# Kernel tuning notes

Hardware: AMD Instinct MI355X
Metric: run time of the kernel (lower is better)

## Reference

```python
import jax, jax.numpy as jnp
import numpy as np

BS, C, H, W = 64, 3, 512, 512
DROP_PIX = 0.3          # fraction of pixels dropped
NOISE_STD = 0.1         # gaussian multiplicative noise std
RNG_SEED = 42           # internal forward randomness (torch RNG analog)


def setup_inputs() -> dict:
    key = jax.random.key(0)
    x = jax.random.normal(key, (BS, C, H, W), dtype=jnp.float32)
    return {"x": x}


def reference(x):
    bs, c, h, w = x.shape
    hw = h * w
    len_keep = int(hw * (1.0 - DROP_PIX))
    k_mask, k_noise = jax.random.split(jax.random.key(RNG_SEED))

    # Per-sample random permutation of pixel indices, keep first len_keep.
    # argsort of iid uniforms == uniformly random permutation (all bs at once,
    # replacing the Python loop + per-iteration randperm of the original).
    u = jax.random.uniform(k_mask, (bs, hw))
    keep_idx = jnp.argsort(u, axis=1)[:, :len_keep]          # [bs, len_keep]
    mask = jnp.zeros((bs, hw), dtype=x.dtype)
    mask = mask.at[jnp.arange(bs)[:, None], keep_idx].set(1.0)
    mask = mask.reshape(bs, 1, h, w)

    # drop_type == 'zeros'
    x = x * mask

    # additive_noise: gaussian multiplicative noise (real-valued branch)
    noise = jax.random.normal(k_noise, x.shape, dtype=x.dtype) * NOISE_STD + 1.0
    x = x * noise
    return x, mask
```

## Files before the change

kernel.cpp:

```cpp
#include <hip/hip_runtime.h>

typedef unsigned int u32;
typedef unsigned long long u64;
typedef unsigned char u8;

__host__ __device__ __forceinline__ void tf2x32(u32 k0, u32 k1, u32 x0, u32 x1,
                                                u32& o0, u32& o1)
{
    const u32 ks2 = k0 ^ k1 ^ 0x1BD11BDAu;
    x0 += k0; x1 += k1;
#define TF_R(r) { x0 += x1; x1 = (x1 << (r)) | (x1 >> (32 - (r))); x1 ^= x0; }
    TF_R(13) TF_R(15) TF_R(26) TF_R(6)
    x0 += k1; x1 += ks2 + 1u;
    TF_R(17) TF_R(29) TF_R(16) TF_R(24)
    x0 += ks2; x1 += k0 + 2u;
    TF_R(13) TF_R(15) TF_R(26) TF_R(6)
    x0 += k0; x1 += k1 + 3u;
    TF_R(17) TF_R(29) TF_R(16) TF_R(24)
    x0 += k1; x1 += ks2 + 4u;
    TF_R(13) TF_R(15) TF_R(26) TF_R(6)
    x0 += ks2; x1 += k0 + 5u;
#undef TF_R
    o0 = x0; o1 = x1;
}

__device__ __forceinline__ u32 rbits(u32 k0, u32 k1, u32 e)
{
    u32 o0, o1; tf2x32(k0, k1, 0u, e, o0, o1); return o0 ^ o1;
}

#define HW        262144u
#define PMASK     262143u
#define KEEP      183500u
#define NX        50331648u
#define NM        16777216u
#define NWORD     524288u
#define LO_F      (-0.99999994039535522461f)

#define WLO       5806464u
#define WWIDTH    131072u
#define NBIN      4096
#define ROWCAP    6144
#define BLKCAP    512

#define BITM_B    (NWORD * 4u)
#define CAND_B    (64u * ROWCAP * 8u)
#define WS_BYTES  (BITM_B + CAND_B)

__device__ u32 g_bitm[NWORD];
__device__ u64 g_cand[64 * ROWCAP];
__device__ u32 g_cnts[128];

__device__ __forceinline__ float noise_from_bits(u32 bits)
{
    float f  = __uint_as_float((bits >> 9) | 0x3F800000u) - 1.0f;
    float un = fmaf(f, 2.0f, LO_F);
    un = fmaxf(LO_F, un);
    float w = -__logf(fmaf(-un, un, 1.0f));
    float p;
    if (w < 5.0f) {
        w -= 2.5f;
        p = 2.81022636e-08f;
        p = fmaf(p, w, 3.43273939e-07f);
        p = fmaf(p, w, -3.5233877e-06f);
        p = fmaf(p, w, -4.39150654e-06f);
        p = fmaf(p, w, 0.00021858087f);
        p = fmaf(p, w, -0.00125372503f);
        p = fmaf(p, w, -0.00417768164f);
        p = fmaf(p, w, 0.246640727f);
        p = fmaf(p, w, 1.50140941f);
    } else {
        w = __fsqrt_rn(w) - 3.0f;
        p = -0.000200214257f;
        p = fmaf(p, w, 0.000100950558f);
        p = fmaf(p, w, 0.00134934322f);
        p = fmaf(p, w, -0.00367342844f);
        p = fmaf(p, w, 0.00573950773f);
        p = fmaf(p, w, -0.0076224613f);
        p = fmaf(p, w, 0.00943887047f);
        p = fmaf(p, w, 1.00167406f);
        p = fmaf(p, w, 2.83297682f);
    }
    float ei = p * un;
    return fmaf(1.41421356f * ei, 0.1f, 1.0f);
}

__global__ __launch_bounds__(256) void k1_scan(u32 mk0, u32 mk1,
                                               u32* __restrict__ bitm,
                                               u64* __restrict__ cand)
{
    __shared__ u64 s_cand[BLKCAP];
    __shared__ u32 s_cnt, s_below, s_base;
    const int t = threadIdx.x;
    const u32 l = (u32)t & 63u;
    const u32 w = (u32)t >> 6;
    const u32 blk = blockIdx.x;
    const u32 row = blk >> 4;
    const u32 base = blk << 14;
    if (t == 0) { s_cnt = 0; s_below = 0; }
    __syncthreads();
    u32 below = 0;
#pragma unroll 1
    for (int i = 0; i < 16; ++i) {
        const u32 base0 = base + ((u32)i << 10) + (w << 8);
        u64 bal[4];
#pragma unroll
        for (int j = 0; j < 4; ++j) {
            u32 e = base0 + ((u32)j << 6) + l;
            u32 m = rbits(mk0, mk1, e) >> 9;
            u32 d = m - WLO;
            below += d >> 31;
            bal[j] = __ballot((int)(d >> 31));
            if (d < WWIDTH) {
                u32 pos = atomicAdd(&s_cnt, 1u);
                if (pos < BLKCAP) s_cand[pos] = ((u64)m << 18) | (u64)(e & PMASK);
            }
        }
        if (l < 8u) {
            u32 qi = l >> 1;
            u64 b = (qi == 0u) ? bal[0] : (qi == 1u) ? bal[1]
                  : (qi == 2u) ? bal[2] : bal[3];
            u32 wv = (l & 1u) ? (u32)(b >> 32) : (u32)b;
            bitm[(base0 >> 5) + l] = wv;
        }
    }
    atomicAdd(&s_below, below);
    __syncthreads();
    u32 cnt = s_cnt; if (cnt > BLKCAP) cnt = BLKCAP;
    if (t == 0) {
        atomicAdd(&g_cnts[row], s_below);
        s_base = atomicAdd(&g_cnts[64 + row], cnt);
    }
    __syncthreads();
    u32 gbase = s_base;
    for (u32 i = (u32)t; i < cnt; i += 256u) {
        u32 gi = gbase + i;
        if (gi < ROWCAP) cand[row * ROWCAP + gi] = s_cand[i];
    }
}

__global__ __launch_bounds__(256) void k2_select(const u64* __restrict__ cand,
                                                 u32* __restrict__ bitm)
{
    __shared__ u32 h[NBIN];
    __shared__ u32 sh[258];
    __shared__ u64 tie[64];
    __shared__ u32 tiecnt;
    __shared__ u64 s_kst;
    const int t = threadIdx.x;
    const u32 row = blockIdx.x;
    u32 n = g_cnts[64 + row]; if (n > ROWCAP) n = ROWCAP;
    u32 below = g_cnts[row];
    u32 r = KEEP - below;
#pragma unroll
    for (int i = 0; i < NBIN / 256; ++i) h[t + (i << 8)] = 0;
    if (t == 0) tiecnt = 0;
    __syncthreads();
    const u64* rc = cand + row * ROWCAP;
    for (u32 i = (u32)t; i < n; i += 256u) {
        u32 m = (u32)(rc[i] >> 18);
        atomicAdd(&h[(m - WLO) >> 5], 1u);
    }
    __syncthreads();
    u32 v[16]; u32 s = 0;
#pragma unroll
    for (int i = 0; i < 16; ++i) { v[i] = h[t * 16 + i]; s += v[i]; }
    sh[t] = s;
    __syncthreads();
    if (t == 0) {
        u32 run = 0; u32 c = 0;
        for (; c < 255u; ++c) { u32 cs = sh[c]; if (run + cs >= r) break; run += cs; }
        sh[256] = c; sh[257] = run;
    }
    __syncthreads();
    u32 c = sh[256];
    if (t == (int)c) {
        u32 run = sh[257];
        u32 b = (u32)t * 16u + 15u; u32 r2 = r - run;
#pragma unroll
        for (int i = 0; i < 16; ++i) {
            if (run + v[i] >= r) { b = (u32)t * 16u + (u32)i; r2 = r - run; break; }
            run += v[i];
        }
        sh[256] = b; sh[257] = r2;
    }
    __syncthreads();
    u32 bstar = sh[256], r2 = sh[257];
    u32 mlo = WLO + (bstar << 5), mhi = mlo + 32u;
    for (u32 i = (u32)t; i < n; i += 256u) {
        u64 k = rc[i];
        u32 m = (u32)(k >> 18);
        if (m >= mlo && m < mhi) {
            u32 pos = atomicAdd(&tiecnt, 1u);
            if (pos < 64u) tie[pos] = k;
        }
    }
    __syncthreads();
    if (t == 0) {
        u32 cnt = tiecnt; if (cnt > 64u) cnt = 64u;
        if (r2 > cnt) r2 = cnt;
        u64 kst = 0;
        for (u32 it = 0; it < r2; ++it) {
            u64 mn = ~0ull; u32 mi = 0;
            for (u32 i2 = 0; i2 < cnt; ++i2) if (tie[i2] < mn) { mn = tie[i2]; mi = i2; }
            kst = mn; tie[mi] = ~0ull;
        }
        s_kst = kst;
    }
    __syncthreads();
    u64 kst = s_kst;
    for (u32 i = (u32)t; i < n; i += 256u) {
        u64 k = rc[i];
        if (k <= kst) {
            u32 p = (u32)k & PMASK;
            atomicOr(&bitm[(row << 13) + (p >> 5)], 1u << (p & 31u));
        }
    }
    if (t == 0) {
        g_cnts[row] = 0;
        g_cnts[64 + row] = 0;
    }
}

__global__ __launch_bounds__(256) void k34_final(const float4* __restrict__ x4,
                                                 float4* __restrict__ out4,
                                                 float4* __restrict__ mask4,
                                                 const u32* __restrict__ bitm,
                                                 u32 nk0, u32 nk1)
{
    u32 tid = blockIdx.x * 256u + threadIdx.x;
    u32 wrd = bitm[tid >> 3];
    u32 nib = wrd >> ((tid & 7u) << 2);
    float4 mk;
    mk.x = (nib & 1u) ? 1.0f : 0.0f;
    mk.y = (nib & 2u) ? 1.0f : 0.0f;
    mk.z = (nib & 4u) ? 1.0f : 0.0f;
    mk.w = (nib & 8u) ? 1.0f : 0.0f;
    mask4[tid] = mk;

    u32 row = tid >> 16;
    u32 p = (tid << 2) & PMASK;
    u32 b3 = row * 3u;
#pragma unroll
    for (u32 cc = 0; cc < 3u; ++cc) {
        u32 en = ((b3 + cc) << 18) | p;
        float4 xv = x4[en >> 2];
        float4 r;
        r.x = (xv.x * mk.x) * noise_from_bits(rbits(nk0, nk1, en));
        r.y = (xv.y * mk.y) * noise_from_bits(rbits(nk0, nk1, en + 1u));
        r.z = (xv.z * mk.z) * noise_from_bits(rbits(nk0, nk1, en + 2u));
        r.w = (xv.w * mk.w) * noise_from_bits(rbits(nk0, nk1, en + 3u));
        out4[en >> 2] = r;
    }
}

extern "C" void kernel_launch(void* const* d_in, const int* in_sizes, int n_in,
                              void* d_out, int out_size, void* d_ws, size_t ws_size,
                              hipStream_t stream) {
    const float* x = (const float*)d_in[0];
    float* xout = (float*)d_out;
    float* maskf = xout + NX;

    u32 mk0, mk1, nk0, nk1;
    tf2x32(0u, 42u, 0u, 0u, mk0, mk1);
    tf2x32(0u, 42u, 0u, 1u, nk0, nk1);

    u32* bitm; u64* cand;
    if (d_ws != nullptr && ws_size >= (size_t)WS_BYTES) {
        u8* wsp = (u8*)d_ws;
        bitm = (u32*)wsp;
        cand = (u64*)(wsp + BITM_B);
    } else {
        hipGetSymbolAddress((void**)&bitm, HIP_SYMBOL(g_bitm));
        hipGetSymbolAddress((void**)&cand, HIP_SYMBOL(g_cand));
    }

    k1_scan<<<1024, 256, 0, stream>>>(mk0, mk1, bitm, cand);
    k2_select<<<64, 256, 0, stream>>>(cand, bitm);
    k34_final<<<16384, 256, 0, stream>>>((const float4*)x, (float4*)xout,
                                         (float4*)maskf, bitm, nk0, nk1);
    (void)in_sizes; (void)n_in; (void)out_size;
}
```

Before: 475.1 us.

## Write float mask in scan/select kernels and use nontemporal loads/stores in final

The float mask output is now written directly by the scan kernel (below-threshold pixels) and by the select kernel (chosen tie candidates), so the final kernel no longer writes it. The final kernel also switches to nontemporal vector loads and stores for x and the output. This spreads the mask write traffic into the earlier, compute-bound RNG scan and aims to cut cache pollution in the streaming kernel. In exchange, the scan kernel issues scalar 4-byte stores, and the select kernel adds scattered stores.

New measurement: 510.7 us. +7.5%, slower.

```diff
diff --git a/kernel.cpp b/kernel.cpp
--- a/kernel.cpp
+++ b/kernel.cpp
@@ -3,6 +3,7 @@
 typedef unsigned int u32;
 typedef unsigned long long u64;
 typedef unsigned char u8;
+typedef float f32x4 __attribute__((ext_vector_type(4)));
 
 __host__ __device__ __forceinline__ void tf2x32(u32 k0, u32 k1, u32 x0, u32 x1,
                                                 u32& o0, u32& o1)
@@ -87,7 +88,8 @@
 
 __global__ __launch_bounds__(256) void k1_scan(u32 mk0, u32 mk1,
                                                u32* __restrict__ bitm,
-                                               u64* __restrict__ cand)
+                                               u64* __restrict__ cand,
+                                               float* __restrict__ maskf)
 {
     __shared__ u64 s_cand[BLKCAP];
     __shared__ u32 s_cnt, s_below, s_base;
@@ -109,8 +111,10 @@
             u32 e = base0 + ((u32)j << 6) + l;
             u32 m = rbits(mk0, mk1, e) >> 9;
             u32 d = m - WLO;
-            below += d >> 31;
-            bal[j] = __ballot((int)(d >> 31));
+            u32 blo = d >> 31;
+            below += blo;
+            bal[j] = __ballot((int)blo);
+            __builtin_nontemporal_store(blo ? 1.0f : 0.0f, &maskf[e]);
             if (d < WWIDTH) {
                 u32 pos = atomicAdd(&s_cnt, 1u);
                 if (pos < BLKCAP) s_cand[pos] = ((u64)m << 18) | (u64)(e & PMASK);
@@ -140,7 +144,8 @@
 }
 
 __global__ __launch_bounds__(256) void k2_select(const u64* __restrict__ cand,
-                                                 u32* __restrict__ bitm)
+                                                 u32* __restrict__ bitm,
+                                                 float* __restrict__ maskf)
 {
     __shared__ u32 h[NBIN];
     __shared__ u32 sh[258];
@@ -214,6 +219,7 @@
         if (k <= kst) {
             u32 p = (u32)k & PMASK;
             atomicOr(&bitm[(row << 13) + (p >> 5)], 1u << (p & 31u));
+            maskf[(row << 18) | p] = 1.0f;
         }
     }
     if (t == 0) {
@@ -222,21 +228,18 @@
     }
 }
 
-__global__ __launch_bounds__(256) void k34_final(const float4* __restrict__ x4,
-                                                 float4* __restrict__ out4,
-                                                 float4* __restrict__ mask4,
+__global__ __launch_bounds__(256) void k34_final(const f32x4* __restrict__ x4,
+                                                 f32x4* __restrict__ out4,
                                                  const u32* __restrict__ bitm,
                                                  u32 nk0, u32 nk1)
 {
     u32 tid = blockIdx.x * 256u + threadIdx.x;
     u32 wrd = bitm[tid >> 3];
     u32 nib = wrd >> ((tid & 7u) << 2);
-    float4 mk;
-    mk.x = (nib & 1u) ? 1.0f : 0.0f;
-    mk.y = (nib & 2u) ? 1.0f : 0.0f;
-    mk.z = (nib & 4u) ? 1.0f : 0.0f;
-    mk.w = (nib & 8u) ? 1.0f : 0.0f;
-    mask4[tid] = mk;
+    float mx = (nib & 1u) ? 1.0f : 0.0f;
+    float my = (nib & 2u) ? 1.0f : 0.0f;
+    float mz = (nib & 4u) ? 1.0f : 0.0f;
+    float mw = (nib & 8u) ? 1.0f : 0.0f;
 
     u32 row = tid >> 16;
     u32 p = (tid << 2) & PMASK;
@@ -244,13 +247,13 @@
 #pragma unroll
     for (u32 cc = 0; cc < 3u; ++cc) {
         u32 en = ((b3 + cc) << 18) | p;
-        float4 xv = x4[en >> 2];
-        float4 r;
-        r.x = (xv.x * mk.x) * noise_from_bits(rbits(nk0, nk1, en));
-        r.y = (xv.y * mk.y) * noise_from_bits(rbits(nk0, nk1, en + 1u));
-        r.z = (xv.z * mk.z) * noise_from_bits(rbits(nk0, nk1, en + 2u));
-        r.w = (xv.w * mk.w) * noise_from_bits(rbits(nk0, nk1, en + 3u));
-        out4[en >> 2] = r;
+        f32x4 xv = __builtin_nontemporal_load(&x4[en >> 2]);
+        f32x4 r;
+        r.x = (xv.x * mx) * noise_from_bits(rbits(nk0, nk1, en));
+        r.y = (xv.y * my) * noise_from_bits(rbits(nk0, nk1, en + 1u));
+        r.z = (xv.z * mz) * noise_from_bits(rbits(nk0, nk1, en + 2u));
+        r.w = (xv.w * mw) * noise_from_bits(rbits(nk0, nk1, en + 3u));
+        __builtin_nontemporal_store(r, &out4[en >> 2]);
     }
 }
 
@@ -275,9 +278,9 @@
         hipGetSymbolAddress((void**)&cand, HIP_SYMBOL(g_cand));
     }
 
-    k1_scan<<<1024, 256, 0, stream>>>(mk0, mk1, bitm, cand);
-    k2_select<<<64, 256, 0, stream>>>(cand, bitm);
-    k34_final<<<16384, 256, 0, stream>>>((const float4*)x, (float4*)xout,
-                                         (float4*)maskf, bitm, nk0, nk1);
+    k1_scan<<<1024, 256, 0, stream>>>(mk0, mk1, bitm, cand, maskf);
+    k2_select<<<64, 256, 0, stream>>>(cand, bitm, maskf);
+    k34_final<<<49152 / 3, 256, 0, stream>>>((const f32x4*)x, (f32x4*)xout,
+                                             bitm, nk0, nk1);
     (void)in_sizes; (void)n_in; (void)out_size;
 }
```

## Fuse mask scan with noise output, patch boundary candidates in select kernel

Applied to the files above, without the earlier changes.

Merges the mask-generating scan and the final noise/multiply pass into one kernel that writes mask and output directly, using only pixels definitely below the threshold window. The select kernel then writes mask=1 and recomputes output for the few boundary candidates it keeps. This removes the bitmap intermediate, its global round trip and one launch. The cost is extra scattered writes in the small select kernel and a smaller per-block candidate buffer (BLKCAP 256 instead of 512) that could overflow.

Measured after the change: 527.7 us. +11.1%, slower.

```diff
diff --git a/kernel.cpp b/kernel.cpp
--- a/kernel.cpp
+++ b/kernel.cpp
@@ -3,6 +3,7 @@
 typedef unsigned int u32;
 typedef unsigned long long u64;
 typedef unsigned char u8;
+typedef float f32x4 __attribute__((ext_vector_type(4)));
 
 __host__ __device__ __forceinline__ void tf2x32(u32 k0, u32 k1, u32 x0, u32 x1,
                                                 u32& o0, u32& o1)
@@ -34,20 +35,17 @@
 #define KEEP      183500u
 #define NX        50331648u
 #define NM        16777216u
-#define NWORD     524288u
 #define LO_F      (-0.99999994039535522461f)
 
 #define WLO       5806464u
 #define WWIDTH    131072u
 #define NBIN      4096
 #define ROWCAP    6144
-#define BLKCAP    512
-
-#define BITM_B    (NWORD * 4u)
+#define BLKCAP    256
+
 #define CAND_B    (64u * ROWCAP * 8u)
-#define WS_BYTES  (BITM_B + CAND_B)
-
-__device__ u32 g_bitm[NWORD];
+#define WS_BYTES  CAND_B
+
 __device__ u64 g_cand[64 * ROWCAP];
 __device__ u32 g_cnts[128];
 
@@ -85,43 +83,53 @@
     return fmaf(1.41421356f * ei, 0.1f, 1.0f);
 }
 
-__global__ __launch_bounds__(256) void k1_scan(u32 mk0, u32 mk1,
-                                               u32* __restrict__ bitm,
-                                               u64* __restrict__ cand)
+__global__ __launch_bounds__(256) void kA_fused(u32 mk0, u32 mk1, u32 nk0, u32 nk1,
+                                                const f32x4* __restrict__ x4,
+                                                f32x4* __restrict__ out4,
+                                                f32x4* __restrict__ mask4,
+                                                u64* __restrict__ cand)
 {
     __shared__ u64 s_cand[BLKCAP];
     __shared__ u32 s_cnt, s_below, s_base;
     const int t = threadIdx.x;
-    const u32 l = (u32)t & 63u;
-    const u32 w = (u32)t >> 6;
     const u32 blk = blockIdx.x;
-    const u32 row = blk >> 4;
-    const u32 base = blk << 14;
+    const u32 row = blk >> 6;
+    const u32 qbase = blk << 10;
     if (t == 0) { s_cnt = 0; s_below = 0; }
     __syncthreads();
     u32 below = 0;
+    const u32 b3 = row * 3u;
 #pragma unroll 1
-    for (int i = 0; i < 16; ++i) {
-        const u32 base0 = base + ((u32)i << 10) + (w << 8);
-        u64 bal[4];
-#pragma unroll
-        for (int j = 0; j < 4; ++j) {
-            u32 e = base0 + ((u32)j << 6) + l;
-            u32 m = rbits(mk0, mk1, e) >> 9;
-            u32 d = m - WLO;
-            below += d >> 31;
-            bal[j] = __ballot((int)(d >> 31));
-            if (d < WWIDTH) {
-                u32 pos = atomicAdd(&s_cnt, 1u);
-                if (pos < BLKCAP) s_cand[pos] = ((u64)m << 18) | (u64)(e & PMASK);
-            }
-        }
-        if (l < 8u) {
-            u32 qi = l >> 1;
-            u64 b = (qi == 0u) ? bal[0] : (qi == 1u) ? bal[1]
-                  : (qi == 2u) ? bal[2] : bal[3];
-            u32 wv = (l & 1u) ? (u32)(b >> 32) : (u32)b;
-            bitm[(base0 >> 5) + l] = wv;
+    for (int j = 0; j < 4; ++j) {
+        u32 q = qbase + ((u32)j << 8) + (u32)t;
+        u32 e = q << 2;
+        u32 p = e & PMASK;
+        u32 m0 = rbits(mk0, mk1, e)      >> 9;
+        u32 m1 = rbits(mk0, mk1, e + 1u) >> 9;
+        u32 m2 = rbits(mk0, mk1, e + 2u) >> 9;
+        u32 m3 = rbits(mk0, mk1, e + 3u) >> 9;
+        u32 d0 = m0 - WLO, d1 = m1 - WLO, d2 = m2 - WLO, d3 = m3 - WLO;
+        below += (d0 >> 31) + (d1 >> 31) + (d2 >> 31) + (d3 >> 31);
+        f32x4 mk;
+        mk.x = (d0 >> 31) ? 1.0f : 0.0f;
+        mk.y = (d1 >> 31) ? 1.0f : 0.0f;
+        mk.z = (d2 >> 31) ? 1.0f : 0.0f;
+        mk.w = (d3 >> 31) ? 1.0f : 0.0f;
+        mask4[q] = mk;
+        if (d0 < WWIDTH) { u32 pos = atomicAdd(&s_cnt, 1u); if (pos < BLKCAP) s_cand[pos] = ((u64)m0 << 18) | (u64)(p); }
+        if (d1 < WWIDTH) { u32 pos = atomicAdd(&s_cnt, 1u); if (pos < BLKCAP) s_cand[pos] = ((u64)m1 << 18) | (u64)(p + 1u); }
+        if (d2 < WWIDTH) { u32 pos = atomicAdd(&s_cnt, 1u); if (pos < BLKCAP) s_cand[pos] = ((u64)m2 << 18) | (u64)(p + 2u); }
+        if (d3 < WWIDTH) { u32 pos = atomicAdd(&s_cnt, 1u); if (pos < BLKCAP) s_cand[pos] = ((u64)m3 << 18) | (u64)(p + 3u); }
+#pragma unroll
+        for (u32 cc = 0; cc < 3u; ++cc) {
+            u32 en = ((b3 + cc) << 18) | p;
+            f32x4 xv = x4[en >> 2];
+            f32x4 r;
+            r.x = (xv.x * mk.x) * noise_from_bits(rbits(nk0, nk1, en));
+            r.y = (xv.y * mk.y) * noise_from_bits(rbits(nk0, nk1, en + 1u));
+            r.z = (xv.z * mk.z) * noise_from_bits(rbits(nk0, nk1, en + 2u));
+            r.w = (xv.w * mk.w) * noise_from_bits(rbits(nk0, nk1, en + 3u));
+            out4[en >> 2] = r;
         }
     }
     atomicAdd(&s_below, below);
@@ -139,8 +147,11 @@
     }
 }
 
-__global__ __launch_bounds__(256) void k2_select(const u64* __restrict__ cand,
-                                                 u32* __restrict__ bitm)
+__global__ __launch_bounds__(256) void kB_select(const u64* __restrict__ cand,
+                                                 const float* __restrict__ x,
+                                                 float* __restrict__ out,
+                                                 float* __restrict__ maskf,
+                                                 u32 nk0, u32 nk1)
 {
     __shared__ u32 h[NBIN];
     __shared__ u32 sh[258];
@@ -209,48 +220,22 @@
     }
     __syncthreads();
     u64 kst = s_kst;
+    const u32 b3 = row * 3u;
     for (u32 i = (u32)t; i < n; i += 256u) {
         u64 k = rc[i];
         if (k <= kst) {
             u32 p = (u32)k & PMASK;
-            atomicOr(&bitm[(row << 13) + (p >> 5)], 1u << (p & 31u));
+            maskf[(row << 18) | p] = 1.0f;
+#pragma unroll
+            for (u32 cc = 0; cc < 3u; ++cc) {
+                u32 en = ((b3 + cc) << 18) | p;
+                out[en] = x[en] * noise_from_bits(rbits(nk0, nk1, en));
+            }
         }
     }
     if (t == 0) {
         g_cnts[row] = 0;
         g_cnts[64 + row] = 0;
-    }
-}
-
-__global__ __launch_bounds__(256) void k34_final(const float4* __restrict__ x4,
-                                                 float4* __restrict__ out4,
-                                                 float4* __restrict__ mask4,
-                                                 const u32* __restrict__ bitm,
-                                                 u32 nk0, u32 nk1)
-{
-    u32 tid = blockIdx.x * 256u + threadIdx.x;
-    u32 wrd = bitm[tid >> 3];
-    u32 nib = wrd >> ((tid & 7u) << 2);
-    float4 mk;
-    mk.x = (nib & 1u) ? 1.0f : 0.0f;
-    mk.y = (nib & 2u) ? 1.0f : 0.0f;
-    mk.z = (nib & 4u) ? 1.0f : 0.0f;
-    mk.w = (nib & 8u) ? 1.0f : 0.0f;
-    mask4[tid] = mk;
-
-    u32 row = tid >> 16;
-    u32 p = (tid << 2) & PMASK;
-    u32 b3 = row * 3u;
-#pragma unroll
-    for (u32 cc = 0; cc < 3u; ++cc) {
-        u32 en = ((b3 + cc) << 18) | p;
-        float4 xv = x4[en >> 2];
-        float4 r;
-        r.x = (xv.x * mk.x) * noise_from_bits(rbits(nk0, nk1, en));
-        r.y = (xv.y * mk.y) * noise_from_bits(rbits(nk0, nk1, en + 1u));
-        r.z = (xv.z * mk.z) * noise_from_bits(rbits(nk0, nk1, en + 2u));
-        r.w = (xv.w * mk.w) * noise_from_bits(rbits(nk0, nk1, en + 3u));
-        out4[en >> 2] = r;
     }
 }
 
@@ -265,19 +250,16 @@
     tf2x32(0u, 42u, 0u, 0u, mk0, mk1);
     tf2x32(0u, 42u, 0u, 1u, nk0, nk1);
 
-    u32* bitm; u64* cand;
+    u64* cand;
     if (d_ws != nullptr && ws_size >= (size_t)WS_BYTES) {
-        u8* wsp = (u8*)d_ws;
-        bitm = (u32*)wsp;
-        cand = (u64*)(wsp + BITM_B);
+        cand = (u64*)d_ws;
     } else {
-        hipGetSymbolAddress((void**)&bitm, HIP_SYMBOL(g_bitm));
         hipGetSymbolAddress((void**)&cand, HIP_SYMBOL(g_cand));
     }
 
-    k1_scan<<<1024, 256, 0, stream>>>(mk0, mk1, bitm, cand);
-    k2_select<<<64, 256, 0, stream>>>(cand, bitm);
-    k34_final<<<16384, 256, 0, stream>>>((const float4*)x, (float4*)xout,
-                                         (float4*)maskf, bitm, nk0, nk1);
+    kA_fused<<<4096, 256, 0, stream>>>(mk0, mk1, nk0, nk1,
+                                       (const f32x4*)x, (f32x4*)xout,
+                                       (f32x4*)maskf, cand);
+    kB_select<<<64, 256, 0, stream>>>(cand, x, xout, maskf, nk0, nk1);
     (void)in_sizes; (void)n_in; (void)out_size;
 }
```
